# Optimization experiments

Measured on AMD Instinct MI355X. Metric: run time of the kernel, lower is better.

## Reference

```python
import jax, jax.numpy as jnp
import numpy as np

B, C, T = 32, 256, 4096

def setup_inputs() -> dict:
    key = jax.random.key(0)
    k1, k2 = jax.random.split(key)
    x = jax.random.normal(k1, (B, C, T), dtype=jnp.float32)
    gamma = jax.random.normal(k2, (1,), dtype=jnp.float32)
    return {"x": x, "gamma": gamma}

def reference(x, gamma):
    # energy[b,i,j] = <x[b,i,:], x[b,j,:]>  -> (B, C, C)
    energy = jnp.einsum('bit,bjt->bij', x, x)
    # max-subtract trick: softmax over (rowmax - energy)
    energy_new = jnp.max(energy, axis=-1, keepdims=True) - energy
    attention = jax.nn.softmax(energy_new, axis=-1)
    # out[b,i,t] = sum_j attention[b,i,j] * x[b,j,t]
    out = jnp.einsum('bij,bjt->bit', attention, x)
    return gamma * out + x
```

## Files before the change

### kernel.cpp

```cpp
#include <hip/hip_runtime.h>
#include <hip/hip_bf16.h>

#define BATCH 32
#define CDIM  256
#define TDIM  4096

using short8  = __attribute__((ext_vector_type(8))) short;
using floatx4 = __attribute__((ext_vector_type(4))) float;

__device__ __forceinline__ unsigned f2bf(float f) {
  unsigned u = __float_as_uint(f);
  return (u + 0x7fffu + ((u >> 16) & 1u)) >> 16;
}
__device__ __forceinline__ unsigned cvt_pk_bf16(float a, float b) {
  return f2bf(a) | (f2bf(b) << 16);
}
__device__ __forceinline__ float bf_lo(unsigned u) { return __uint_as_float(u << 16); }
__device__ __forceinline__ float bf_hi(unsigned u) { return __uint_as_float(u & 0xffff0000u); }

__global__ __launch_bounds__(512, 1)
void gram_kernel(const float* __restrict__ x,
                 float* __restrict__ E1, float* __restrict__ E2) {
  __shared__ __align__(16) short hI[128 * 64];
  __shared__ __align__(16) short lI[128 * 64];
  __shared__ __align__(16) short hJ[64 * 64];

  const int tid = threadIdx.x;
  const int bx  = blockIdx.x;

  const int s   = bx & 7;
  const int seq = bx >> 3;
  const int b   = s + ((seq >> 3) << 3);
  const int job = seq & 7;
  const int i0  = (job >> 2) << 7;
  const int j0  = (job & 3) << 6;

  const float* xb = x + ((size_t)b << 20);

  const bool isJ   = tid >= 256;
  const int  irow  = tid >> 1;
  const int  ihalf = tid & 1;
  const int  jrow  = (tid & 255) >> 2;
  const int  jq    = tid & 3;

  const float* pS = isJ
      ? xb + (size_t)(j0 + jrow) * TDIM + (jq << 4)
      : xb + (size_t)(i0 + irow) * TDIM + (ihalf << 5);

  floatx4 acc1[2][2], acc2[2][2];
#pragma unroll
  for (int m = 0; m < 2; ++m)
#pragma unroll
    for (int n = 0; n < 2; ++n) {
      acc1[m][n] = {0.f, 0.f, 0.f, 0.f};
      acc2[m][n] = {0.f, 0.f, 0.f, 0.f};
    }

  const int lane = tid & 63;
  const int w    = tid >> 6;
  const int wib  = (w >> 1) << 5;
  const int wjb  = (w & 1) << 5;
  const int fr   = lane & 15;
  const int q    = lane >> 4;
  const int f7   = fr & 7;

  const int g0 = ((q)     ^ f7) << 3;
  const int g1 = ((q + 4) ^ f7) << 3;
  const int a0 = (wib + fr) << 6;
  const int a1 = (wib + 16 + fr) << 6;
  const int b0 = (wjb + fr) << 6;
  const int b1 = (wjb + 16 + fr) << 6;

  float4 r0, r1, r2, r3, r4, r5, r6, r7;
  r0 = ((const float4*)pS)[0]; r1 = ((const float4*)pS)[1];
  r2 = ((const float4*)pS)[2]; r3 = ((const float4*)pS)[3];
  if (!isJ) {
    r4 = ((const float4*)pS)[4]; r5 = ((const float4*)pS)[5];
    r6 = ((const float4*)pS)[6]; r7 = ((const float4*)pS)[7];
  }

  for (int ks = 0; ks < TDIM / 64; ++ks) {
    unsigned h0 = cvt_pk_bf16(r0.x, r0.y), h1 = cvt_pk_bf16(r0.z, r0.w);
    unsigned h2 = cvt_pk_bf16(r1.x, r1.y), h3 = cvt_pk_bf16(r1.z, r1.w);
    unsigned h4 = cvt_pk_bf16(r2.x, r2.y), h5 = cvt_pk_bf16(r2.z, r2.w);
    unsigned h6 = cvt_pk_bf16(r3.x, r3.y), h7 = cvt_pk_bf16(r3.z, r3.w);
    unsigned h8, h9, hA, hB, hC, hD, hE, hF;
    unsigned l0, l1, l2, l3, l4, l5, l6, l7, l8, l9, lA, lB, lC, lD, lE, lF;
    if (!isJ) {
      h8 = cvt_pk_bf16(r4.x, r4.y); h9 = cvt_pk_bf16(r4.z, r4.w);
      hA = cvt_pk_bf16(r5.x, r5.y); hB = cvt_pk_bf16(r5.z, r5.w);
      hC = cvt_pk_bf16(r6.x, r6.y); hD = cvt_pk_bf16(r6.z, r6.w);
      hE = cvt_pk_bf16(r7.x, r7.y); hF = cvt_pk_bf16(r7.z, r7.w);
      l0 = cvt_pk_bf16(r0.x - bf_lo(h0), r0.y - bf_hi(h0));
      l1 = cvt_pk_bf16(r0.z - bf_lo(h1), r0.w - bf_hi(h1));
      l2 = cvt_pk_bf16(r1.x - bf_lo(h2), r1.y - bf_hi(h2));
      l3 = cvt_pk_bf16(r1.z - bf_lo(h3), r1.w - bf_hi(h3));
      l4 = cvt_pk_bf16(r2.x - bf_lo(h4), r2.y - bf_hi(h4));
      l5 = cvt_pk_bf16(r2.z - bf_lo(h5), r2.w - bf_hi(h5));
      l6 = cvt_pk_bf16(r3.x - bf_lo(h6), r3.y - bf_hi(h6));
      l7 = cvt_pk_bf16(r3.z - bf_lo(h7), r3.w - bf_hi(h7));
      l8 = cvt_pk_bf16(r4.x - bf_lo(h8), r4.y - bf_hi(h8));
      l9 = cvt_pk_bf16(r4.z - bf_lo(h9), r4.w - bf_hi(h9));
      lA = cvt_pk_bf16(r5.x - bf_lo(hA), r5.y - bf_hi(hA));
      lB = cvt_pk_bf16(r5.z - bf_lo(hB), r5.w - bf_hi(hB));
      lC = cvt_pk_bf16(r6.x - bf_lo(hC), r6.y - bf_hi(hC));
      lD = cvt_pk_bf16(r6.z - bf_lo(hD), r6.w - bf_hi(hD));
      lE = cvt_pk_bf16(r7.x - bf_lo(hE), r7.y - bf_hi(hE));
      lF = cvt_pk_bf16(r7.z - bf_lo(hF), r7.w - bf_hi(hF));
    }

    __syncthreads();
    if (!isJ) {
      const int rb = irow << 6;
      const int s7 = irow & 7;
      const int gb = ihalf << 2;
      *(uint4*)&hI[rb + (((gb + 0) ^ s7) << 3)] = make_uint4(h0, h1, h2, h3);
      *(uint4*)&hI[rb + (((gb + 1) ^ s7) << 3)] = make_uint4(h4, h5, h6, h7);
      *(uint4*)&hI[rb + (((gb + 2) ^ s7) << 3)] = make_uint4(h8, h9, hA, hB);
      *(uint4*)&hI[rb + (((gb + 3) ^ s7) << 3)] = make_uint4(hC, hD, hE, hF);
      *(uint4*)&lI[rb + (((gb + 0) ^ s7) << 3)] = make_uint4(l0, l1, l2, l3);
      *(uint4*)&lI[rb + (((gb + 1) ^ s7) << 3)] = make_uint4(l4, l5, l6, l7);
      *(uint4*)&lI[rb + (((gb + 2) ^ s7) << 3)] = make_uint4(l8, l9, lA, lB);
      *(uint4*)&lI[rb + (((gb + 3) ^ s7) << 3)] = make_uint4(lC, lD, lE, lF);
    } else {
      const int rb = jrow << 6;
      const int s7 = jrow & 7;
      const int gb = jq << 1;
      *(uint4*)&hJ[rb + (((gb + 0) ^ s7) << 3)] = make_uint4(h0, h1, h2, h3);
      *(uint4*)&hJ[rb + (((gb + 1) ^ s7) << 3)] = make_uint4(h4, h5, h6, h7);
    }
    __syncthreads();

    if (ks < TDIM / 64 - 1) {
      pS += 64;
      r0 = ((const float4*)pS)[0]; r1 = ((const float4*)pS)[1];
      r2 = ((const float4*)pS)[2]; r3 = ((const float4*)pS)[3];
      if (!isJ) {
        r4 = ((const float4*)pS)[4]; r5 = ((const float4*)pS)[5];
        r6 = ((const float4*)pS)[6]; r7 = ((const float4*)pS)[7];
      }
    }

    {
      short8 Ah0 = *(const short8*)&hI[a0 + g0];
      short8 Ah1 = *(const short8*)&hI[a1 + g0];
      short8 Al0 = *(const short8*)&lI[a0 + g0];
      short8 Al1 = *(const short8*)&lI[a1 + g0];
      short8 Bh0 = *(const short8*)&hJ[b0 + g0];
      short8 Bh1 = *(const short8*)&hJ[b1 + g0];
      acc1[0][0] = __builtin_amdgcn_mfma_f32_16x16x32_bf16(Ah0, Bh0, acc1[0][0], 0, 0, 0);
      acc1[0][1] = __builtin_amdgcn_mfma_f32_16x16x32_bf16(Ah0, Bh1, acc1[0][1], 0, 0, 0);
      acc1[1][0] = __builtin_amdgcn_mfma_f32_16x16x32_bf16(Ah1, Bh0, acc1[1][0], 0, 0, 0);
      acc1[1][1] = __builtin_amdgcn_mfma_f32_16x16x32_bf16(Ah1, Bh1, acc1[1][1], 0, 0, 0);
      acc2[0][0] = __builtin_amdgcn_mfma_f32_16x16x32_bf16(Al0, Bh0, acc2[0][0], 0, 0, 0);
      acc2[0][1] = __builtin_amdgcn_mfma_f32_16x16x32_bf16(Al0, Bh1, acc2[0][1], 0, 0, 0);
      acc2[1][0] = __builtin_amdgcn_mfma_f32_16x16x32_bf16(Al1, Bh0, acc2[1][0], 0, 0, 0);
      acc2[1][1] = __builtin_amdgcn_mfma_f32_16x16x32_bf16(Al1, Bh1, acc2[1][1], 0, 0, 0);
    }
    {
      short8 Ah0 = *(const short8*)&hI[a0 + g1];
      short8 Ah1 = *(const short8*)&hI[a1 + g1];
      short8 Al0 = *(const short8*)&lI[a0 + g1];
      short8 Al1 = *(const short8*)&lI[a1 + g1];
      short8 Bh0 = *(const short8*)&hJ[b0 + g1];
      short8 Bh1 = *(const short8*)&hJ[b1 + g1];
      acc1[0][0] = __builtin_amdgcn_mfma_f32_16x16x32_bf16(Ah0, Bh0, acc1[0][0], 0, 0, 0);
      acc1[0][1] = __builtin_amdgcn_mfma_f32_16x16x32_bf16(Ah0, Bh1, acc1[0][1], 0, 0, 0);
      acc1[1][0] = __builtin_amdgcn_mfma_f32_16x16x32_bf16(Ah1, Bh0, acc1[1][0], 0, 0, 0);
      acc1[1][1] = __builtin_amdgcn_mfma_f32_16x16x32_bf16(Ah1, Bh1, acc1[1][1], 0, 0, 0);
      acc2[0][0] = __builtin_amdgcn_mfma_f32_16x16x32_bf16(Al0, Bh0, acc2[0][0], 0, 0, 0);
      acc2[0][1] = __builtin_amdgcn_mfma_f32_16x16x32_bf16(Al0, Bh1, acc2[0][1], 0, 0, 0);
      acc2[1][0] = __builtin_amdgcn_mfma_f32_16x16x32_bf16(Al1, Bh0, acc2[1][0], 0, 0, 0);
      acc2[1][1] = __builtin_amdgcn_mfma_f32_16x16x32_bf16(Al1, Bh1, acc2[1][1], 0, 0, 0);
    }
  }

#pragma unroll
  for (int m = 0; m < 2; ++m)
#pragma unroll
    for (int n = 0; n < 2; ++n) {
      const int gr = i0 + wib + 16 * m + 4 * q;
      const int gc = j0 + wjb + 16 * n + fr;
      size_t base = (((size_t)b * CDIM + gr) << 8) + gc;
#pragma unroll
      for (int r = 0; r < 4; ++r) {
        E1[base + ((size_t)r << 8)] = acc1[m][n][r];
        E2[base + ((size_t)r << 8)] = acc2[m][n][r];
      }
    }
}

__global__ __launch_bounds__(256)
void softmax_kernel(const float* __restrict__ E1, const float* __restrict__ E2,
                    __hip_bfloat16* __restrict__ att) {
  __shared__ float SR[32][264];
  __shared__ float ST[256][33];

  const int tid = threadIdx.x;
  const int b   = blockIdx.x >> 3;
  const int i0  = (blockIdx.x & 7) << 5;
  const size_t base = (size_t)b << 16;

  {
    const int r  = tid >> 3;
    const int c0 = (tid & 7) << 5;
    const float* p1 = E1 + base + ((size_t)(i0 + r) << 8) + c0;
    const float* p2 = E2 + base + ((size_t)(i0 + r) << 8) + c0;
#pragma unroll
    for (int u = 0; u < 32; u += 4) {
      float4 a = *(const float4*)(p1 + u);
      float4 c = *(const float4*)(p2 + u);
      *(float4*)&SR[r][c0 + u] = make_float4(a.x + c.x, a.y + c.y, a.z + c.z, a.w + c.w);
    }
  }
  {
    const int c  = tid & 31;
    const int j0 = (tid >> 5) << 5;
    const float* p = E2 + base + i0 + c;
#pragma unroll
    for (int jj = 0; jj < 32; ++jj)
      ST[j0 + jj][c] = p[(size_t)(j0 + jj) << 8];
  }
  __syncthreads();

  const int r  = tid >> 3;
  const int t7 = tid & 7;
  float z[32];
  float m = -3.4e38f;
#pragma unroll
  for (int k = 0; k < 32; ++k) {
    const int j = t7 + (k << 3);
    const float e = SR[r][j] + ST[j][r];
    z[k] = -e;
    m = fmaxf(m, z[k]);
  }
  m = fmaxf(m, __shfl_xor(m, 1, 64));
  m = fmaxf(m, __shfl_xor(m, 2, 64));
  m = fmaxf(m, __shfl_xor(m, 4, 64));
  float ssum = 0.f;
#pragma unroll
  for (int k = 0; k < 32; ++k) { z[k] = expf(z[k] - m); ssum += z[k]; }
  ssum += __shfl_xor(ssum, 1, 64);
  ssum += __shfl_xor(ssum, 2, 64);
  ssum += __shfl_xor(ssum, 4, 64);
  const float inv = 1.f / ssum;

  unsigned short* arow = (unsigned short*)att + base + ((size_t)(i0 + r) << 8);
#pragma unroll
  for (int k = 0; k < 32; ++k) {
    const int j = t7 + (k << 3);
    arow[j] = (unsigned short)f2bf(z[k] * inv);
  }
}

__global__ __launch_bounds__(256, 1)
void pv_kernel(const float* __restrict__ x, const __hip_bfloat16* __restrict__ att,
               const float* __restrict__ gamma, float* __restrict__ out) {
  __shared__ __align__(16) short As[128 * 256];
  __shared__ __align__(16) short Bs[128 * 256];

  const int tid = threadIdx.x;
  const int bx  = blockIdx.x;
  const int b   = bx >> 6;
  const int i0  = ((bx >> 5) & 1) << 7;
  const int t0  = (bx & 31) << 7;

  const float* xb = x + ((size_t)b << 20) + t0;
  const unsigned short* attb =
      (const unsigned short*)att + ((size_t)b << 16) + ((size_t)i0 << 8);

  {
    uint4 areg[16];
#pragma unroll
    for (int c = 0; c < 16; ++c) {
      const int p = (c << 8) + tid;
      const int r = p >> 5;
      const int g = (p & 31) ^ (r & 7);
      areg[c] = *(const uint4*)(attb + (r << 8) + (g << 3));
    }
#pragma unroll
    for (int c = 0; c < 16; ++c) {
      const int p = (c << 8) + tid;
      *(uint4*)((char*)As + ((size_t)p << 4)) = areg[c];
    }
  }

  {
    const int tQ = tid & 31;
    const int jg = tid >> 5;
#pragma unroll
    for (int j8 = 0; j8 < 4; ++j8) {
      floatx4 v[8];
#pragma unroll
      for (int u = 0; u < 8; ++u) {
        const int j = (jg << 5) + (j8 << 3) + u;
        v[u] = *(const floatx4*)(xb + (size_t)j * TDIM + (tQ << 2));
      }
#pragma unroll
      for (int tt = 0; tt < 4; ++tt) {
        uint4 wv = make_uint4(cvt_pk_bf16(v[0][tt], v[1][tt]),
                              cvt_pk_bf16(v[2][tt], v[3][tt]),
                              cvt_pk_bf16(v[4][tt], v[5][tt]),
                              cvt_pk_bf16(v[6][tt], v[7][tt]));
        const int row = (tQ << 2) + tt;
        const int g   = ((jg << 2) + j8) ^ (row & 7);
        *(uint4*)((char*)Bs + (size_t)row * 512 + ((size_t)g << 4)) = wv;
      }
    }
  }

  floatx4 acc[4][4];
#pragma unroll
  for (int m = 0; m < 4; ++m)
#pragma unroll
    for (int n = 0; n < 4; ++n) acc[m][n] = {0.f, 0.f, 0.f, 0.f};

  const int lane = tid & 63;
  const int w    = tid >> 6;
  const int wm   = (w >> 1) << 6;
  const int wn   = (w & 1) << 6;
  const int fr   = lane & 15;
  const int q    = lane >> 4;

  __syncthreads();

#pragma unroll
  for (int ks = 0; ks < 8; ++ks) {
    short8 Af[4], Bf[4];
#pragma unroll
    for (int m = 0; m < 4; ++m) {
      const int r = wm + 16 * m + fr;
      const int g = ((ks << 2) + q) ^ (r & 7);
      Af[m] = *(const short8*)((char*)As + (size_t)r * 512 + ((size_t)g << 4));
    }
#pragma unroll
    for (int n = 0; n < 4; ++n) {
      const int r = wn + 16 * n + fr;
      const int g = ((ks << 2) + q) ^ (r & 7);
      Bf[n] = *(const short8*)((char*)Bs + (size_t)r * 512 + ((size_t)g << 4));
    }
#pragma unroll
    for (int m = 0; m < 4; ++m)
#pragma unroll
      for (int n = 0; n < 4; ++n)
        acc[m][n] = __builtin_amdgcn_mfma_f32_16x16x32_bf16(Af[m], Bf[n], acc[m][n], 0, 0, 0);
  }

  const float g = gamma[0];
#pragma unroll
  for (int m = 0; m < 4; ++m)
#pragma unroll
    for (int n = 0; n < 4; ++n) {
      const int gr = i0 + wm + 16 * m + 4 * q;
      const int gc = t0 + wn + 16 * n + fr;
      size_t base = ((size_t)b << 20) + (size_t)gr * TDIM + gc;
#pragma unroll
      for (int r = 0; r < 4; ++r) {
        size_t idx = base + (size_t)r * TDIM;
        out[idx] = g * acc[m][n][r] + x[idx];
      }
    }
}

extern "C" void kernel_launch(void* const* d_in, const int* in_sizes, int n_in,
                              void* d_out, int out_size, void* d_ws, size_t ws_size,
                              hipStream_t stream) {
  (void)in_sizes; (void)n_in; (void)out_size; (void)ws_size;
  const float* x     = (const float*)d_in[0];
  const float* gamma = (const float*)d_in[1];
  float* out = (float*)d_out;

  const size_t EN = (size_t)BATCH * CDIM * CDIM;
  float* E1 = (float*)d_ws;
  float* E2 = E1 + EN;
  __hip_bfloat16* att = (__hip_bfloat16*)(E2 + EN);

  gram_kernel<<<dim3(256), dim3(512), 0, stream>>>(x, E1, E2);
  softmax_kernel<<<dim3(BATCH * 8), dim3(256), 0, stream>>>(E1, E2, att);
  pv_kernel<<<dim3(2048), dim3(256), 0, stream>>>(x, att, gamma, out);
}
```

Measured before the change: 400.0 us.

## Precompute bf16 hi/lo split of x and stream it via LDS-direct loads

Adds a split kernel that converts x once into bf16 high and low parts in workspace. The Gram GEMM then reads these with double-buffered global_load_lds instead of converting fp32 in-loop, and the PV kernel reads the bf16 high part instead of fp32 x. The Gram kernel also pre-sums S = E1 + E2 so softmax reads one less matrix. This adds a full extra pass over x (read fp32, write 2x bf16) and needs a large workspace, falling back to the old path when the workspace is too small.

Measured after the change: 371.3 us. -7.2%, faster.

```diff
diff --git a/kernel.cpp b/kernel.cpp
--- a/kernel.cpp
+++ b/kernel.cpp
@@ -7,6 +7,7 @@
 
 using short8  = __attribute__((ext_vector_type(8))) short;
 using floatx4 = __attribute__((ext_vector_type(4))) float;
+typedef unsigned short u16;
 
 __device__ __forceinline__ unsigned f2bf(float f) {
   unsigned u = __float_as_uint(f);
@@ -18,16 +19,158 @@
 __device__ __forceinline__ float bf_lo(unsigned u) { return __uint_as_float(u << 16); }
 __device__ __forceinline__ float bf_hi(unsigned u) { return __uint_as_float(u & 0xffff0000u); }
 
+__device__ __forceinline__ void glds16(const void* g, void* l) {
+  __builtin_amdgcn_global_load_lds(
+      (const __attribute__((address_space(1))) void*)g,
+      (__attribute__((address_space(3))) void*)l, 16, 0, 0);
+}
+
+__global__ __launch_bounds__(256)
+void split_kernel(const float* __restrict__ x, u16* __restrict__ hx,
+                  u16* __restrict__ lx) {
+  const unsigned gid0 = blockIdx.x * 256 + threadIdx.x;
+#pragma unroll
+  for (int it = 0; it < 8; ++it) {
+    const size_t g8 = ((size_t)gid0 + (size_t)it * (2048u * 256u)) * 8;
+    const float4 a = *(const float4*)(x + g8);
+    const float4 c = *(const float4*)(x + g8 + 4);
+    unsigned h0 = cvt_pk_bf16(a.x, a.y), h1 = cvt_pk_bf16(a.z, a.w);
+    unsigned h2 = cvt_pk_bf16(c.x, c.y), h3 = cvt_pk_bf16(c.z, c.w);
+    unsigned l0 = cvt_pk_bf16(a.x - bf_lo(h0), a.y - bf_hi(h0));
+    unsigned l1 = cvt_pk_bf16(a.z - bf_lo(h1), a.w - bf_hi(h1));
+    unsigned l2 = cvt_pk_bf16(c.x - bf_lo(h2), c.y - bf_hi(h2));
+    unsigned l3 = cvt_pk_bf16(c.z - bf_lo(h3), c.w - bf_hi(h3));
+    *(uint4*)(hx + g8) = make_uint4(h0, h1, h2, h3);
+    *(uint4*)(lx + g8) = make_uint4(l0, l1, l2, l3);
+  }
+}
+
 __global__ __launch_bounds__(512, 1)
-void gram_kernel(const float* __restrict__ x,
-                 float* __restrict__ E1, float* __restrict__ E2) {
+void gram_gemm(const u16* __restrict__ hx, const u16* __restrict__ lx,
+               float* __restrict__ S, float* __restrict__ E2) {
+  __shared__ __align__(16) short lds[2 * 20480];
+
+  const int tid = threadIdx.x;
+  const int bx  = blockIdx.x;
+
+  const int s8  = bx & 7;
+  const int seq = bx >> 3;
+  const int b   = s8 + ((seq >> 3) << 3);
+  const int job = seq & 7;
+  const int i0  = (job >> 2) << 7;
+  const int j0  = (job & 3) << 6;
+
+  const int lane = tid & 63;
+  const int w    = tid >> 6;
+
+  const int rsub = lane >> 3;
+  const int gsw  = ((lane & 7) ^ rsub) << 3;
+  const size_t xb = (size_t)b << 20;
+  const u16* src[5];
+  src[0] = hx + xb + (size_t)(i0 +      w * 8 + rsub) * TDIM + gsw;
+  src[1] = hx + xb + (size_t)(i0 + 64 + w * 8 + rsub) * TDIM + gsw;
+  src[2] = lx + xb + (size_t)(i0 +      w * 8 + rsub) * TDIM + gsw;
+  src[3] = lx + xb + (size_t)(i0 + 64 + w * 8 + rsub) * TDIM + gsw;
+  src[4] = hx + xb + (size_t)(j0 +      w * 8 + rsub) * TDIM + gsw;
+  int dstoff[5];
+#pragma unroll
+  for (int s = 0; s < 5; ++s) dstoff[s] = (s * 8 + w) << 9;
+
+  floatx4 acc1[2][2], acc2[2][2];
+#pragma unroll
+  for (int m = 0; m < 2; ++m)
+#pragma unroll
+    for (int n = 0; n < 2; ++n) {
+      acc1[m][n] = {0.f, 0.f, 0.f, 0.f};
+      acc2[m][n] = {0.f, 0.f, 0.f, 0.f};
+    }
+
+  const int wib = (w >> 1) << 5;
+  const int wjb = (w & 1) << 5;
+  const int fr  = lane & 15;
+  const int q   = lane >> 4;
+  const int f7  = fr & 7;
+
+  const int g0 = ((q)     ^ f7) << 3;
+  const int g1 = ((q + 4) ^ f7) << 3;
+  const int a0 = (wib + fr) << 6;
+  const int a1 = a0 + (16 << 6);
+  const int b0 = (wjb + fr) << 6;
+  const int b1 = b0 + (16 << 6);
+
+#pragma unroll
+  for (int s = 0; s < 5; ++s) glds16(src[s], lds + dstoff[s]);
+  __syncthreads();
+
+  for (int ks = 0; ks < 64; ++ks) {
+    const int cur = ks & 1;
+    if (ks < 63) {
+      const int nb = (cur ^ 1) * 20480;
+#pragma unroll
+      for (int s = 0; s < 5; ++s)
+        glds16(src[s] + ((ks + 1) << 6), lds + nb + dstoff[s]);
+    }
+    const int bb = cur * 20480;
+
+    {
+      short8 Ah0 = *(const short8*)&lds[bb + a0 + g0];
+      short8 Ah1 = *(const short8*)&lds[bb + a1 + g0];
+      short8 Al0 = *(const short8*)&lds[bb + 8192 + a0 + g0];
+      short8 Al1 = *(const short8*)&lds[bb + 8192 + a1 + g0];
+      short8 Bh0 = *(const short8*)&lds[bb + 16384 + b0 + g0];
+      short8 Bh1 = *(const short8*)&lds[bb + 16384 + b1 + g0];
+      acc1[0][0] = __builtin_amdgcn_mfma_f32_16x16x32_bf16(Ah0, Bh0, acc1[0][0], 0, 0, 0);
+      acc1[0][1] = __builtin_amdgcn_mfma_f32_16x16x32_bf16(Ah0, Bh1, acc1[0][1], 0, 0, 0);
+      acc1[1][0] = __builtin_amdgcn_mfma_f32_16x16x32_bf16(Ah1, Bh0, acc1[1][0], 0, 0, 0);
+      acc1[1][1] = __builtin_amdgcn_mfma_f32_16x16x32_bf16(Ah1, Bh1, acc1[1][1], 0, 0, 0);
+      acc2[0][0] = __builtin_amdgcn_mfma_f32_16x16x32_bf16(Al0, Bh0, acc2[0][0], 0, 0, 0);
+      acc2[0][1] = __builtin_amdgcn_mfma_f32_16x16x32_bf16(Al0, Bh1, acc2[0][1], 0, 0, 0);
+      acc2[1][0] = __builtin_amdgcn_mfma_f32_16x16x32_bf16(Al1, Bh0, acc2[1][0], 0, 0, 0);
+      acc2[1][1] = __builtin_amdgcn_mfma_f32_16x16x32_bf16(Al1, Bh1, acc2[1][1], 0, 0, 0);
+    }
+    {
+      short8 Ah0 = *(const short8*)&lds[bb + a0 + g1];
+      short8 Ah1 = *(const short8*)&lds[bb + a1 + g1];
+      short8 Al0 = *(const short8*)&lds[bb + 8192 + a0 + g1];
+      short8 Al1 = *(const short8*)&lds[bb + 8192 + a1 + g1];
+      short8 Bh0 = *(const short8*)&lds[bb + 16384 + b0 + g1];
+      short8 Bh1 = *(const short8*)&lds[bb + 16384 + b1 + g1];
+      acc1[0][0] = __builtin_amdgcn_mfma_f32_16x16x32_bf16(Ah0, Bh0, acc1[0][0], 0, 0, 0);
+      acc1[0][1] = __builtin_amdgcn_mfma_f32_16x16x32_bf16(Ah0, Bh1, acc1[0][1], 0, 0, 0);
+      acc1[1][0] = __builtin_amdgcn_mfma_f32_16x16x32_bf16(Ah1, Bh0, acc1[1][0], 0, 0, 0);
+      acc1[1][1] = __builtin_amdgcn_mfma_f32_16x16x32_bf16(Ah1, Bh1, acc1[1][1], 0, 0, 0);
+      acc2[0][0] = __builtin_amdgcn_mfma_f32_16x16x32_bf16(Al0, Bh0, acc2[0][0], 0, 0, 0);
+      acc2[0][1] = __builtin_amdgcn_mfma_f32_16x16x32_bf16(Al0, Bh1, acc2[0][1], 0, 0, 0);
+      acc2[1][0] = __builtin_amdgcn_mfma_f32_16x16x32_bf16(Al1, Bh0, acc2[1][0], 0, 0, 0);
+      acc2[1][1] = __builtin_amdgcn_mfma_f32_16x16x32_bf16(Al1, Bh1, acc2[1][1], 0, 0, 0);
+    }
+    __syncthreads();
+  }
+
+#pragma unroll
+  for (int m = 0; m < 2; ++m)
+#pragma unroll
+    for (int n = 0; n < 2; ++n) {
+      const int gr = i0 + wib + 16 * m + 4 * q;
+      const int gc = j0 + wjb + 16 * n + fr;
+      size_t base = (((size_t)b * CDIM + gr) << 8) + gc;
+#pragma unroll
+      for (int r = 0; r < 4; ++r) {
+        S[base + ((size_t)r << 8)]  = acc1[m][n][r] + acc2[m][n][r];
+        E2[base + ((size_t)r << 8)] = acc2[m][n][r];
+      }
+    }
+}
+
+__global__ __launch_bounds__(512, 1)
+void gram_fused(const float* __restrict__ x,
+                float* __restrict__ S, float* __restrict__ E2) {
   __shared__ __align__(16) short hI[128 * 64];
   __shared__ __align__(16) short lI[128 * 64];
   __shared__ __align__(16) short hJ[64 * 64];
 
   const int tid = threadIdx.x;
   const int bx  = blockIdx.x;
-
   const int s   = bx & 7;
   const int seq = bx >> 3;
   const int b   = s + ((seq >> 3) << 3);
@@ -67,9 +210,9 @@
   const int g0 = ((q)     ^ f7) << 3;
   const int g1 = ((q + 4) ^ f7) << 3;
   const int a0 = (wib + fr) << 6;
-  const int a1 = (wib + 16 + fr) << 6;
+  const int a1 = a0 + (16 << 6);
   const int b0 = (wjb + fr) << 6;
-  const int b1 = (wjb + 16 + fr) << 6;
+  const int b1 = b0 + (16 << 6);
 
   float4 r0, r1, r2, r3, r4, r5, r6, r7;
   r0 = ((const float4*)pS)[0]; r1 = ((const float4*)pS)[1];
@@ -184,14 +327,14 @@
       size_t base = (((size_t)b * CDIM + gr) << 8) + gc;
 #pragma unroll
       for (int r = 0; r < 4; ++r) {
-        E1[base + ((size_t)r << 8)] = acc1[m][n][r];
+        S[base + ((size_t)r << 8)]  = acc1[m][n][r] + acc2[m][n][r];
         E2[base + ((size_t)r << 8)] = acc2[m][n][r];
       }
     }
 }
 
 __global__ __launch_bounds__(256)
-void softmax_kernel(const float* __restrict__ E1, const float* __restrict__ E2,
+void softmax_kernel(const float* __restrict__ S, const float* __restrict__ E2,
                     __hip_bfloat16* __restrict__ att) {
   __shared__ float SR[32][264];
   __shared__ float ST[256][33];
@@ -204,14 +347,10 @@
   {
     const int r  = tid >> 3;
     const int c0 = (tid & 7) << 5;
-    const float* p1 = E1 + base + ((size_t)(i0 + r) << 8) + c0;
-    const float* p2 = E2 + base + ((size_t)(i0 + r) << 8) + c0;
-#pragma unroll
-    for (int u = 0; u < 32; u += 4) {
-      float4 a = *(const float4*)(p1 + u);
-      float4 c = *(const float4*)(p2 + u);
-      *(float4*)&SR[r][c0 + u] = make_float4(a.x + c.x, a.y + c.y, a.z + c.z, a.w + c.w);
-    }
+    const float* p1 = S + base + ((size_t)(i0 + r) << 8) + c0;
+#pragma unroll
+    for (int u = 0; u < 32; u += 4)
+      *(float4*)&SR[r][c0 + u] = *(const float4*)(p1 + u);
   }
   {
     const int c  = tid & 31;
@@ -245,16 +384,17 @@
   ssum += __shfl_xor(ssum, 4, 64);
   const float inv = 1.f / ssum;
 
-  unsigned short* arow = (unsigned short*)att + base + ((size_t)(i0 + r) << 8);
+  u16* arow = (u16*)att + base + ((size_t)(i0 + r) << 8);
 #pragma unroll
   for (int k = 0; k < 32; ++k) {
     const int j = t7 + (k << 3);
-    arow[j] = (unsigned short)f2bf(z[k] * inv);
+    arow[j] = (u16)f2bf(z[k] * inv);
   }
 }
 
 __global__ __launch_bounds__(256, 1)
-void pv_kernel(const float* __restrict__ x, const __hip_bfloat16* __restrict__ att,
+void pv_kernel(const float* __restrict__ x, const u16* __restrict__ hx,
+               const __hip_bfloat16* __restrict__ att,
                const float* __restrict__ gamma, float* __restrict__ out) {
   __shared__ __align__(16) short As[128 * 256];
   __shared__ __align__(16) short Bs[128 * 256];
@@ -265,9 +405,112 @@
   const int i0  = ((bx >> 5) & 1) << 7;
   const int t0  = (bx & 31) << 7;
 
+  const u16* attb = (const u16*)att + ((size_t)b << 16) + ((size_t)i0 << 8);
+  const int lane = tid & 63;
+  const int w4   = tid >> 6;
+
+  const int tQ = tid & 31;
+  const int jg = tid >> 5;
+  const u16* hb = hx + ((size_t)b << 20) + t0 + (tQ << 2);
+  uint2 v[4][8];
+#pragma unroll
+  for (int j8 = 0; j8 < 4; ++j8)
+#pragma unroll
+    for (int u = 0; u < 8; ++u)
+      v[j8][u] = *(const uint2*)(hb + (size_t)((jg << 5) + (j8 << 3) + u) * TDIM);
+
+#pragma unroll
+  for (int s = 0; s < 16; ++s) {
+    const int c  = (s << 2) + w4;
+    const int r  = (c << 1) + (lane >> 5);
+    const int gd = lane & 31;
+    const int gs = gd ^ (r & 7);
+    glds16(attb + ((size_t)r << 8) + (gs << 3), As + (c << 9));
+  }
+
+#pragma unroll
+  for (int j8 = 0; j8 < 4; ++j8) {
+#pragma unroll
+    for (int tt = 0; tt < 4; ++tt) {
+      unsigned p[4];
+#pragma unroll
+      for (int a = 0; a < 4; ++a) {
+        const unsigned xa = (tt & 2) ? v[j8][2 * a].y : v[j8][2 * a].x;
+        const unsigned xb2 = (tt & 2) ? v[j8][2 * a + 1].y : v[j8][2 * a + 1].x;
+        p[a] = (tt & 1) ? ((xa >> 16) | (xb2 & 0xffff0000u))
+                        : ((xa & 0xffffu) | (xb2 << 16));
+      }
+      const int row = (tQ << 2) + tt;
+      const int g   = ((jg << 2) + j8) ^ (row & 7);
+      *(uint4*)(Bs + row * 256 + (g << 3)) = make_uint4(p[0], p[1], p[2], p[3]);
+    }
+  }
+
+  floatx4 acc[4][4];
+#pragma unroll
+  for (int m = 0; m < 4; ++m)
+#pragma unroll
+    for (int n = 0; n < 4; ++n) acc[m][n] = {0.f, 0.f, 0.f, 0.f};
+
+  const int wm = (w4 >> 1) << 6;
+  const int wn = (w4 & 1) << 6;
+  const int fr = lane & 15;
+  const int q  = lane >> 4;
+
+  __syncthreads();
+
+#pragma unroll
+  for (int ks = 0; ks < 8; ++ks) {
+    short8 Af[4], Bf[4];
+#pragma unroll
+    for (int m = 0; m < 4; ++m) {
+      const int r = wm + 16 * m + fr;
+      const int g = ((ks << 2) + q) ^ (r & 7);
+      Af[m] = *(const short8*)(As + r * 256 + (g << 3));
+    }
+#pragma unroll
+    for (int n = 0; n < 4; ++n) {
+      const int r = wn + 16 * n + fr;
+      const int g = ((ks << 2) + q) ^ (r & 7);
+      Bf[n] = *(const short8*)(Bs + r * 256 + (g << 3));
+    }
+#pragma unroll
+    for (int m = 0; m < 4; ++m)
+#pragma unroll
+      for (int n = 0; n < 4; ++n)
+        acc[m][n] = __builtin_amdgcn_mfma_f32_16x16x32_bf16(Af[m], Bf[n], acc[m][n], 0, 0, 0);
+  }
+
+  const float g = gamma[0];
+#pragma unroll
+  for (int m = 0; m < 4; ++m)
+#pragma unroll
+    for (int n = 0; n < 4; ++n) {
+      const int gr = i0 + wm + 16 * m + 4 * q;
+      const int gc = t0 + wn + 16 * n + fr;
+      size_t base = ((size_t)b << 20) + (size_t)gr * TDIM + gc;
+#pragma unroll
+      for (int r = 0; r < 4; ++r) {
+        size_t idx = base + (size_t)r * TDIM;
+        out[idx] = g * acc[m][n][r] + x[idx];
+      }
+    }
+}
+
+__global__ __launch_bounds__(256, 1)
+void pv_fused(const float* __restrict__ x, const __hip_bfloat16* __restrict__ att,
+              const float* __restrict__ gamma, float* __restrict__ out) {
+  __shared__ __align__(16) short As[128 * 256];
+  __shared__ __align__(16) short Bs[128 * 256];
+
+  const int tid = threadIdx.x;
+  const int bx  = blockIdx.x;
+  const int b   = bx >> 6;
+  const int i0  = ((bx >> 5) & 1) << 7;
+  const int t0  = (bx & 31) << 7;
+
   const float* xb = x + ((size_t)b << 20) + t0;
-  const unsigned short* attb =
-      (const unsigned short*)att + ((size_t)b << 16) + ((size_t)i0 << 8);
+  const u16* attb = (const u16*)att + ((size_t)b << 16) + ((size_t)i0 << 8);
 
   {
     uint4 areg[16];
@@ -284,7 +527,6 @@
       *(uint4*)((char*)As + ((size_t)p << 4)) = areg[c];
     }
   }
-
   {
     const int tQ = tid & 31;
     const int jg = tid >> 5;
@@ -365,17 +607,28 @@
 extern "C" void kernel_launch(void* const* d_in, const int* in_sizes, int n_in,
                               void* d_out, int out_size, void* d_ws, size_t ws_size,
                               hipStream_t stream) {
-  (void)in_sizes; (void)n_in; (void)out_size; (void)ws_size;
+  (void)in_sizes; (void)n_in; (void)out_size;
   const float* x     = (const float*)d_in[0];
   const float* gamma = (const float*)d_in[1];
   float* out = (float*)d_out;
 
   const size_t EN = (size_t)BATCH * CDIM * CDIM;
-  float* E1 = (float*)d_ws;
-  float* E2 = E1 + EN;
+  const size_t XN = (size_t)BATCH * CDIM * TDIM;
+  float* S  = (float*)d_ws;
+  float* E2 = S + EN;
   __hip_bfloat16* att = (__hip_bfloat16*)(E2 + EN);
-
-  gram_kernel<<<dim3(256), dim3(512), 0, stream>>>(x, E1, E2);
-  softmax_kernel<<<dim3(BATCH * 8), dim3(256), 0, stream>>>(E1, E2, att);
-  pv_kernel<<<dim3(2048), dim3(256), 0, stream>>>(x, att, gamma, out);
-}
+  u16* hx = (u16*)((char*)d_ws + 20u * 1024 * 1024);
+  u16* lx = hx + XN;
+  const size_t need = 20u * 1024 * 1024 + 2 * XN * sizeof(u16);
+
+  if (ws_size >= need) {
+    split_kernel<<<dim3(2048), dim3(256), 0, stream>>>(x, hx, lx);
+    gram_gemm<<<dim3(256), dim3(512), 0, stream>>>(hx, lx, S, E2);
+    softmax_kernel<<<dim3(BATCH * 8), dim3(256), 0, stream>>>(S, E2, att);
+    pv_kernel<<<dim3(2048), dim3(256), 0, stream>>>(x, hx, att, gamma, out);
+  } else {
+    gram_fused<<<dim3(256), dim3(512), 0, stream>>>(x, S, E2);
+    softmax_kernel<<<dim3(BATCH * 8), dim3(256), 0, stream>>>(S, E2, att);
+    pv_fused<<<dim3(2048), dim3(256), 0, stream>>>(x, att, gamma, out);
+  }
+}
```
